# Kernel tuning notes

Hardware: AMD Instinct MI355X
Metric: run time of the kernel (lower is better)

## Reference

```python
import jax, jax.numpy as jnp
import numpy as np

B = 16384
D = 20          # input_size == hidden_size
L = 1000        # num_layers (all hidden layers, uniform 20x20)


def setup_inputs() -> dict:
    key = jax.random.key(0)
    kx, kw, kb, kwo, kbo = jax.random.split(key, 5)
    scale = 1.0 / np.sqrt(D)
    x = jax.random.normal(kx, (B, D), dtype=jnp.float32)
    # 1000 stacked Linear(20,20) layers; torch Linear weight is (out, in)
    W = jax.random.normal(kw, (L, D, D), dtype=jnp.float32) * scale
    b = jax.random.normal(kb, (L, D), dtype=jnp.float32) * scale
    # final Linear(20, 1)
    W_out = jax.random.normal(kwo, (1, D), dtype=jnp.float32) * scale
    b_out = jax.random.normal(kbo, (1,), dtype=jnp.float32) * scale
    return {"x": x, "W": W, "b": b, "W_out": W_out, "b_out": b_out}


def reference(x, W, b, W_out, b_out):
    def step(h, wb):
        w, bb = wb  # w: [D, D] (out, in), bb: [D]
        h = jax.nn.sigmoid(h @ w.T + bb)  # [B, D]
        return h, None

    h, _ = jax.lax.scan(step, x, (W, b))
    # final Linear(D, 1) + sigmoid
    out = jax.nn.sigmoid(h @ W_out.T + b_out)  # [B, 1]
    return out
```

## Files before the change

### kernel.cpp

```cpp
#include <hip/hip_runtime.h>

#define LOG2E 1.44269504088896340736f

typedef __attribute__((ext_vector_type(8))) short short8;
typedef __attribute__((ext_vector_type(4))) float f32x4;
typedef __attribute__((ext_vector_type(2))) float f32x2;

constexpr int CL       = 10;
constexpr int LAYER_BY = 2048;
constexpr int CHUNK_BY = CL * LAYER_BY;
constexpr int CHUNK_V4 = CHUNK_BY / 16;
constexpr int V4_PER_T = CHUNK_V4 / 256;

__device__ __forceinline__ int slot_pos(int h, int e) {
    return (e < 4) ? (4 * h + e) : (16 + 4 * h + (e - 4));
}

__device__ __forceinline__ unsigned short f32_to_bf16_rne(float f) {
    unsigned u = __builtin_bit_cast(unsigned, f);
    unsigned r = 0x7fffu + ((u >> 16) & 1u);
    return (unsigned short)((u + r) >> 16);
}

__global__ void prepack(const float* __restrict__ W, const float* __restrict__ b,
                        unsigned int* __restrict__ wstream, int L)
{
    const int l    = blockIdx.x;
    const int t    = threadIdx.x >> 6;
    const int lane = threadIdx.x & 63;
    const int n    = t * 16 + (lane & 15);
    const int h    = lane >> 4;
    unsigned int words[4];
#pragma unroll
    for (int d = 0; d < 4; ++d) {
        unsigned short halves[2];
#pragma unroll
        for (int half = 0; half < 2; ++half) {
            int e   = d * 2 + half;
            int pos = slot_pos(h, e);
            float v = 0.f;
            if (n < 20) {
                if (pos < 20)       v = W[(size_t)l * 400 + n * 20 + pos];
                else if (pos == 20) v = b[(size_t)l * 20 + n];
            }
            halves[half] = f32_to_bf16_rne(v * 0.5f);
        }
        words[d] = (unsigned)halves[0] | ((unsigned)halves[1] << 16);
    }
    unsigned int* dst = wstream + ((size_t)l * LAYER_BY + t * 1024 + lane * 16) / 4;
    dst[0] = words[0]; dst[1] = words[1]; dst[2] = words[2]; dst[3] = words[3];
}

__device__ __forceinline__ unsigned cvt_pk_bf16(float lo, float hi) {
    unsigned r;
    asm("v_cvt_pk_bf16_f32 %0, %1, %2" : "=v"(r) : "v"(lo), "v"(hi));
    return r;
}

__device__ __forceinline__ short8 finalize_B(unsigned p0, unsigned p1,
                                             unsigned p2, unsigned p3, int h) {
    if (h != 0) { p2 = (h == 1) ? 0x00003F80u : 0u; p3 = 0u; }
    union { unsigned u[4]; short8 s; } cv;
    cv.u[0] = p0; cv.u[1] = p1; cv.u[2] = p2; cv.u[3] = p3;
    return cv.s;
}

__device__ __forceinline__ f32x2 make2(float v) { f32x2 r; r.x = v; r.y = v; return r; }

__device__ __forceinline__ f32x2 pade_sig(f32x2 x) {
    f32x2 u = x * x;
    f32x2 n = (u * make2(0.5f) + make2(52.5f)) * u + make2(472.5f);
    f32x2 d = (u * make2(15.0f) + make2(420.0f)) * u + make2(945.0f);
    f32x2 r;
    r.x = __builtin_amdgcn_rcpf(d.x);
    r.y = __builtin_amdgcn_rcpf(d.y);
    return (x * n) * r + make2(0.5f);
}

__device__ __forceinline__ float sigm(float z) {
    return __builtin_amdgcn_rcpf(1.f + __builtin_amdgcn_exp2f(-LOG2E * z));
}

__global__ __launch_bounds__(256, 1) void mann_mfma(
    const float* __restrict__ x, const unsigned int* __restrict__ wstream,
    const float* __restrict__ Wout, const float* __restrict__ bout,
    float* __restrict__ out, int B, int L)
{
    __shared__ unsigned char lds[2 * CHUNK_BY];

    const int tid  = threadIdx.x;
    const int lane = tid & 63;
    const int c16  = lane & 15;
    const int h    = lane >> 4;
    const int w    = (blockIdx.x * 256 + tid) >> 6;
    const int row  = w * 16 + c16;

    const float4 xa = *reinterpret_cast<const float4*>(x + (size_t)row * 20 + 4 * h);
    const float4 xb = *reinterpret_cast<const float4*>(x + (size_t)row * 20 + 16);
    short8 Bf = finalize_B(cvt_pk_bf16(xa.x, xa.y), cvt_pk_bf16(xa.z, xa.w),
                           cvt_pk_bf16(xb.x, xb.y), cvt_pk_bf16(xb.z, xb.w), h);

    float4 sreg[V4_PER_T];
    auto stage_load = [&](int c) {
        const float4* g = reinterpret_cast<const float4*>(wstream) + (size_t)c * CHUNK_V4;
#pragma unroll
        for (int j = 0; j < V4_PER_T; ++j) sreg[j] = g[j * 256 + tid];
    };
    auto stage_write = [&](int bufi) {
        float4* d = reinterpret_cast<float4*>(lds + bufi * CHUNK_BY);
#pragma unroll
        for (int j = 0; j < V4_PER_T; ++j) d[j * 256 + tid] = sreg[j];
    };

    const unsigned lbase = (unsigned)(uintptr_t)&lds[0];

    stage_load(0); stage_write(0); __syncthreads();

    short8 a0A, a1A, a0B, a1B;
    auto issue_A = [&](unsigned addr, short8& t0, short8& t1) {
        asm volatile("ds_read_b128 %0, %1 offset:0"    : "=v"(t0) : "v"(addr));
        asm volatile("ds_read_b128 %0, %1 offset:1024" : "=v"(t1) : "v"(addr));
    };
    issue_A(lbase + lane * 16, a0A, a1A);

    const f32x4 zero = {0.f, 0.f, 0.f, 0.f};
    f32x2 q0, q1, q2, q3;

    const int NC = L / CL;
    for (int c = 0; c < NC; ++c) {
        if (c + 1 < NC) stage_load(c + 1);
        const unsigned cb = lbase + (c & 1) * CHUNK_BY + lane * 16;
#pragma unroll
        for (int ll = 0; ll < CL; ++ll) {
            const bool even = (ll & 1) == 0;
            short8& c0 = even ? a0A : a0B;
            short8& c1 = even ? a1A : a1B;
            short8& n0 = even ? a0B : a0A;
            short8& n1 = even ? a1B : a1A;
            asm volatile("s_waitcnt lgkmcnt(0)" ::: "memory");
            __builtin_amdgcn_sched_barrier(0);
            if (ll + 1 < CL) issue_A(cb + (ll + 1) * LAYER_BY, n0, n1);
            f32x4 acc0 = __builtin_amdgcn_mfma_f32_16x16x32_bf16(c0, Bf, zero, 0, 0, 0);
            f32x4 acc1 = __builtin_amdgcn_mfma_f32_16x16x32_bf16(c1, Bf, zero, 0, 0, 0);
            q0.x = acc0[0]; q0.y = acc0[1];
            q1.x = acc0[2]; q1.y = acc0[3];
            q2.x = acc1[0]; q2.y = acc1[1];
            q3.x = acc1[2]; q3.y = acc1[3];
            q0 = pade_sig(q0); q1 = pade_sig(q1);
            q2 = pade_sig(q2); q3 = pade_sig(q3);
            Bf = finalize_B(cvt_pk_bf16(q0.x, q0.y), cvt_pk_bf16(q1.x, q1.y),
                            cvt_pk_bf16(q2.x, q2.y), cvt_pk_bf16(q3.x, q3.y), h);
        }
        if (c + 1 < NC) {
            stage_write((c + 1) & 1);
            __syncthreads();
            issue_A(lbase + ((c + 1) & 1) * CHUNK_BY + lane * 16, a0A, a1A);
        }
    }

    const float4 woa = *reinterpret_cast<const float4*>(Wout + 4 * h);
    const float4 wob = *reinterpret_cast<const float4*>(Wout + 16);
    float part = q0.x * woa.x + q0.y * woa.y + q1.x * woa.z + q1.y * woa.w;
    const float m = (h == 0) ? 1.f : 0.f;
    part += m * (q2.x * wob.x + q2.y * wob.y + q3.x * wob.z + q3.y * wob.w);
    part += __shfl_xor(part, 16, 64);
    part += __shfl_xor(part, 32, 64);
    if (h == 0) out[row] = sigm(part + bout[0]);
}

extern "C" void kernel_launch(void* const* d_in, const int* in_sizes, int n_in,
                              void* d_out, int out_size, void* d_ws, size_t ws_size,
                              hipStream_t stream) {
    const float* x    = (const float*)d_in[0];
    const float* W    = (const float*)d_in[1];
    const float* b    = (const float*)d_in[2];
    const float* Wout = (const float*)d_in[3];
    const float* bout = (const float*)d_in[4];
    float* out = (float*)d_out;

    const int B = in_sizes[0] / 20;
    const int L = in_sizes[1] / 400;

    unsigned int* wstream = (unsigned int*)d_ws;

    prepack<<<L, 128, 0, stream>>>(W, b, wstream, L);

    const int grid = B / 64;
    mann_mfma<<<grid, 256, 0, stream>>>(x, wstream, Wout, bout, out, B, L);
}
```

Before: 278.4 us.

## Stream layer weights directly from global memory with register prefetch, dropping LDS staging

Replaces the double-buffered LDS chunk staging (global→register→LDS with block-wide barriers every 10 layers) with direct per-wave global loads of each layer's packed weights, prefetched two layers ahead in registers. This removes the __syncthreads and LDS write/read traffic. In exchange every wave fetches weights from L2/L1 on the critical path, and global load latency has to be hidden by only a two-layer prefetch distance. The per-layer MFMA/sigmoid math is moved into a helper function and is otherwise unchanged.

After: 387.9 us. +39.3%, slower.

```diff
diff --git a/kernel.cpp b/kernel.cpp
--- a/kernel.cpp
+++ b/kernel.cpp
@@ -6,11 +6,7 @@
 typedef __attribute__((ext_vector_type(4))) float f32x4;
 typedef __attribute__((ext_vector_type(2))) float f32x2;
 
-constexpr int CL       = 10;
-constexpr int LAYER_BY = 2048;
-constexpr int CHUNK_BY = CL * LAYER_BY;
-constexpr int CHUNK_V4 = CHUNK_BY / 16;
-constexpr int V4_PER_T = CHUNK_V4 / 256;
+constexpr int LAYER_S8 = 128;
 
 __device__ __forceinline__ int slot_pos(int h, int e) {
     return (e < 4) ? (4 * h + e) : (16 + 4 * h + (e - 4));
@@ -47,7 +43,7 @@
         }
         words[d] = (unsigned)halves[0] | ((unsigned)halves[1] << 16);
     }
-    unsigned int* dst = wstream + ((size_t)l * LAYER_BY + t * 1024 + lane * 16) / 4;
+    unsigned int* dst = wstream + ((size_t)l * 2048 + t * 1024 + lane * 16) / 4;
     dst[0] = words[0]; dst[1] = words[1]; dst[2] = words[2]; dst[3] = words[3];
 }
 
@@ -81,13 +77,26 @@
     return __builtin_amdgcn_rcpf(1.f + __builtin_amdgcn_exp2f(-LOG2E * z));
 }
 
+__device__ __forceinline__ void layer_step(const short8& c0, const short8& c1,
+                                           short8& Bf, f32x2 (&q)[4], int h) {
+    const f32x4 zero = {0.f, 0.f, 0.f, 0.f};
+    f32x4 acc0 = __builtin_amdgcn_mfma_f32_16x16x32_bf16(c0, Bf, zero, 0, 0, 0);
+    f32x4 acc1 = __builtin_amdgcn_mfma_f32_16x16x32_bf16(c1, Bf, zero, 0, 0, 0);
+    q[0].x = acc0[0]; q[0].y = acc0[1];
+    q[1].x = acc0[2]; q[1].y = acc0[3];
+    q[2].x = acc1[0]; q[2].y = acc1[1];
+    q[3].x = acc1[2]; q[3].y = acc1[3];
+    q[0] = pade_sig(q[0]); q[1] = pade_sig(q[1]);
+    q[2] = pade_sig(q[2]); q[3] = pade_sig(q[3]);
+    Bf = finalize_B(cvt_pk_bf16(q[0].x, q[0].y), cvt_pk_bf16(q[1].x, q[1].y),
+                    cvt_pk_bf16(q[2].x, q[2].y), cvt_pk_bf16(q[3].x, q[3].y), h);
+}
+
 __global__ __launch_bounds__(256, 1) void mann_mfma(
     const float* __restrict__ x, const unsigned int* __restrict__ wstream,
     const float* __restrict__ Wout, const float* __restrict__ bout,
     float* __restrict__ out, int B, int L)
 {
-    __shared__ unsigned char lds[2 * CHUNK_BY];
-
     const int tid  = threadIdx.x;
     const int lane = tid & 63;
     const int c16  = lane & 15;
@@ -100,69 +109,30 @@
     short8 Bf = finalize_B(cvt_pk_bf16(xa.x, xa.y), cvt_pk_bf16(xa.z, xa.w),
                            cvt_pk_bf16(xb.x, xb.y), cvt_pk_bf16(xb.z, xb.w), h);
 
-    float4 sreg[V4_PER_T];
-    auto stage_load = [&](int c) {
-        const float4* g = reinterpret_cast<const float4*>(wstream) + (size_t)c * CHUNK_V4;
-#pragma unroll
-        for (int j = 0; j < V4_PER_T; ++j) sreg[j] = g[j * 256 + tid];
-    };
-    auto stage_write = [&](int bufi) {
-        float4* d = reinterpret_cast<float4*>(lds + bufi * CHUNK_BY);
-#pragma unroll
-        for (int j = 0; j < V4_PER_T; ++j) d[j * 256 + tid] = sreg[j];
-    };
+    const short8* __restrict__ wp = reinterpret_cast<const short8*>(wstream);
 
-    const unsigned lbase = (unsigned)(uintptr_t)&lds[0];
+    short8 c0 = wp[0 * LAYER_S8 + lane];
+    short8 c1 = wp[0 * LAYER_S8 + 64 + lane];
+    short8 n0 = wp[1 * LAYER_S8 + lane];
+    short8 n1 = wp[1 * LAYER_S8 + 64 + lane];
 
-    stage_load(0); stage_write(0); __syncthreads();
+    f32x2 q[4];
 
-    short8 a0A, a1A, a0B, a1B;
-    auto issue_A = [&](unsigned addr, short8& t0, short8& t1) {
-        asm volatile("ds_read_b128 %0, %1 offset:0"    : "=v"(t0) : "v"(addr));
-        asm volatile("ds_read_b128 %0, %1 offset:1024" : "=v"(t1) : "v"(addr));
-    };
-    issue_A(lbase + lane * 16, a0A, a1A);
-
-    const f32x4 zero = {0.f, 0.f, 0.f, 0.f};
-    f32x2 q0, q1, q2, q3;
-
-    const int NC = L / CL;
-    for (int c = 0; c < NC; ++c) {
-        if (c + 1 < NC) stage_load(c + 1);
-        const unsigned cb = lbase + (c & 1) * CHUNK_BY + lane * 16;
-#pragma unroll
-        for (int ll = 0; ll < CL; ++ll) {
-            const bool even = (ll & 1) == 0;
-            short8& c0 = even ? a0A : a0B;
-            short8& c1 = even ? a1A : a1B;
-            short8& n0 = even ? a0B : a0A;
-            short8& n1 = even ? a1B : a1A;
-            asm volatile("s_waitcnt lgkmcnt(0)" ::: "memory");
-            __builtin_amdgcn_sched_barrier(0);
-            if (ll + 1 < CL) issue_A(cb + (ll + 1) * LAYER_BY, n0, n1);
-            f32x4 acc0 = __builtin_amdgcn_mfma_f32_16x16x32_bf16(c0, Bf, zero, 0, 0, 0);
-            f32x4 acc1 = __builtin_amdgcn_mfma_f32_16x16x32_bf16(c1, Bf, zero, 0, 0, 0);
-            q0.x = acc0[0]; q0.y = acc0[1];
-            q1.x = acc0[2]; q1.y = acc0[3];
-            q2.x = acc1[0]; q2.y = acc1[1];
-            q3.x = acc1[2]; q3.y = acc1[3];
-            q0 = pade_sig(q0); q1 = pade_sig(q1);
-            q2 = pade_sig(q2); q3 = pade_sig(q3);
-            Bf = finalize_B(cvt_pk_bf16(q0.x, q0.y), cvt_pk_bf16(q1.x, q1.y),
-                            cvt_pk_bf16(q2.x, q2.y), cvt_pk_bf16(q3.x, q3.y), h);
-        }
-        if (c + 1 < NC) {
-            stage_write((c + 1) & 1);
-            __syncthreads();
-            issue_A(lbase + ((c + 1) & 1) * CHUNK_BY + lane * 16, a0A, a1A);
-        }
+#pragma unroll 4
+    for (int l = 0; l < L; ++l) {
+        const int lp = (l + 2 < L) ? (l + 2) : (L - 1);
+        short8 p0 = wp[(size_t)lp * LAYER_S8 + lane];
+        short8 p1 = wp[(size_t)lp * LAYER_S8 + 64 + lane];
+        layer_step(c0, c1, Bf, q, h);
+        c0 = n0; c1 = n1;
+        n0 = p0; n1 = p1;
     }
 
     const float4 woa = *reinterpret_cast<const float4*>(Wout + 4 * h);
     const float4 wob = *reinterpret_cast<const float4*>(Wout + 16);
-    float part = q0.x * woa.x + q0.y * woa.y + q1.x * woa.z + q1.y * woa.w;
+    float part = q[0].x * woa.x + q[0].y * woa.y + q[1].x * woa.z + q[1].y * woa.w;
     const float m = (h == 0) ? 1.f : 0.f;
-    part += m * (q2.x * wob.x + q2.y * wob.y + q3.x * wob.z + q3.y * wob.w);
+    part += m * (q[2].x * wob.x + q[2].y * wob.y + q[3].x * wob.z + q[3].y * wob.w);
     part += __shfl_xor(part, 16, 64);
     part += __shfl_xor(part, 32, 64);
     if (h == 0) out[row] = sigm(part + bout[0]);
```
